# Performance work log

Hardware: AMD Instinct MI355X
Metric: run time of the kernel (lower is better)

## Reference

```python
import jax, jax.numpy as jnp
import numpy as np

N_GRAPHS = 256
NODES_PER_GRAPH = 64
N_NODES = N_GRAPHS * NODES_PER_GRAPH  # 16384
IN_F = 128
OUT_F = 128
N_HEADS = 16


def setup_inputs() -> dict:
    key = jax.random.key(0)
    k1, k2, k3, k4 = jax.random.split(key, 4)
    inputs = jax.random.normal(k1, (N_NODES, IN_F), dtype=jnp.float32)
    # fixed equal-sized graphs so sum(n_node) == N_NODES exactly
    n_node = jnp.full((N_GRAPHS,), NODES_PER_GRAPH, dtype=jnp.int32)
    head = jax.random.randint(k2, (N_GRAPHS,), 0, N_HEADS, dtype=jnp.int32)
    # lecun_normal-like init: std = 1/sqrt(fan_in)
    kernel = jax.random.normal(k3, (N_HEADS, IN_F, OUT_F), dtype=jnp.float32) * (1.0 / np.sqrt(IN_F))
    bias = jax.random.normal(k4, (N_HEADS, OUT_F), dtype=jnp.float32) * 0.02
    return {"inputs": inputs, "n_node": n_node, "head": head, "kernel": kernel, "bias": bias}


def reference(inputs, n_node, head, kernel, bias):
    # per-node head index: repeat each graph's head over its nodes
    node_head = jnp.repeat(head, n_node, total_repeat_length=inputs.shape[0])  # [N]
    k = kernel[node_head]                       # [N, in, out] (gathered per-node weights)
    y = jnp.einsum('bi,bio->bo', inputs, k)     # [N, out]
    y = y + bias[node_head]                     # [N, out]
    return y
```

## Files before the change

kernel.cpp:

```cpp
#include <hip/hip_runtime.h>
#include <hip/hip_bf16.h>

#define NG   256
#define NPG  64
#define INF  128
#define OUTF 128
#define NH   16

#define LDSK 136

typedef __attribute__((ext_vector_type(8))) short bf16x8;
typedef __attribute__((ext_vector_type(4))) float f32x4;

__device__ __forceinline__ ushort f2bf(float f) {
    union { float f; unsigned int i; } c; c.f = f;
    unsigned int r = c.i + 0x7fffu + ((c.i >> 16) & 1u);
    return (ushort)(r >> 16);
}

__global__ __launch_bounds__(512) void mhl_fused_kernel(
    const float* __restrict__ X,
    const int*   __restrict__ head,
    const float* __restrict__ W,
    const float* __restrict__ bias,
    float*       __restrict__ Y)
{
    __shared__ ushort Wl[OUTF * LDSK];

    int g = (int)blockIdx.x;
    int h = head[g];
    int t = (int)threadIdx.x;

    {
        int k  = t >> 2;
        int c0 = (t & 3) * 32;
        const float* src = W + h * (INF * OUTF) + k * OUTF + c0;
#pragma unroll
        for (int j = 0; j < 32; j += 4) {
            float4 v = *(const float4*)(src + j);
            Wl[(c0 + j + 0) * LDSK + k] = f2bf(v.x);
            Wl[(c0 + j + 1) * LDSK + k] = f2bf(v.y);
            Wl[(c0 + j + 2) * LDSK + k] = f2bf(v.z);
            Wl[(c0 + j + 3) * LDSK + k] = f2bf(v.w);
        }
    }
    __syncthreads();

    int wave = t >> 6;
    int lane = t & 63;
    int quad = lane >> 4;
    int l16  = lane & 15;

    int mrow = (wave & 3) * 16;
    int ncol = (wave >> 2) * 64;

    const float* Xg = X + (g * NPG + mrow + l16) * INF + quad * 8;
    bf16x8 a[4];
#pragma unroll
    for (int kt = 0; kt < 4; ++kt) {
        float v[8] __attribute__((aligned(16)));
        *(float4*)(&v[0]) = *(const float4*)(Xg + kt * 32);
        *(float4*)(&v[4]) = *(const float4*)(Xg + kt * 32 + 4);
#pragma unroll
        for (int j = 0; j < 8; ++j) a[kt][j] = (short)f2bf(v[j]);
    }

    f32x4 acc[4];
#pragma unroll
    for (int nt = 0; nt < 4; ++nt) acc[nt] = (f32x4){0.f, 0.f, 0.f, 0.f};

#pragma unroll
    for (int nt = 0; nt < 4; ++nt) {
        const ushort* Wn = &Wl[(ncol + nt * 16 + l16) * LDSK + quad * 8];
#pragma unroll
        for (int kt = 0; kt < 4; ++kt) {
            bf16x8 b = *(const bf16x8*)(Wn + kt * 32);
            acc[nt] = __builtin_amdgcn_mfma_f32_16x16x32_bf16(a[kt], b, acc[nt], 0, 0, 0);
        }
    }

    float* Yg = Y + (g * NPG + mrow) * OUTF + ncol;
#pragma unroll
    for (int nt = 0; nt < 4; ++nt) {
        float bv = bias[h * OUTF + ncol + nt * 16 + l16];
#pragma unroll
        for (int r = 0; r < 4; ++r)
            Yg[(quad * 4 + r) * OUTF + nt * 16 + l16] = acc[nt][r] + bv;
    }
}

extern "C" void kernel_launch(void* const* d_in, const int* in_sizes, int n_in,
                              void* d_out, int out_size, void* d_ws, size_t ws_size,
                              hipStream_t stream) {
    const float* X    = (const float*)d_in[0];
    const int*   head = (const int*)d_in[2];
    const float* W    = (const float*)d_in[3];
    const float* bias = (const float*)d_in[4];
    float* Y = (float*)d_out;

    mhl_fused_kernel<<<NG, 512, 0, stream>>>(X, head, W, bias, Y);
}
```

Before: 72.06 us.

## Split each graph across two blocks by output half and pack bf16 pairs in LDS

Each graph is now handled by two 256-thread blocks, each covering 64 output columns, so the grid doubles to 512 blocks and each block stages only half of the head's weight matrix. The weight staging now converts two adjacent k rows at once and writes packed 32-bit pairs to LDS, halving the number of LDS stores and reducing bank conflicts on the transposed writes. The aim is better CU occupancy on a GPU with many CUs and less per-block staging latency. The cost is that each block re-reads its X rows, so X is loaded twice per graph.

Measured after the change: 72.32 us. About the same (+0.4%).

```diff
diff --git a/kernel.cpp b/kernel.cpp
--- a/kernel.cpp
+++ b/kernel.cpp
@@ -18,30 +18,38 @@
     return (ushort)(r >> 16);
 }
 
-__global__ __launch_bounds__(512) void mhl_fused_kernel(
+__global__ __launch_bounds__(256) void mhl_fused_kernel(
     const float* __restrict__ X,
     const int*   __restrict__ head,
     const float* __restrict__ W,
     const float* __restrict__ bias,
     float*       __restrict__ Y)
 {
-    __shared__ ushort Wl[OUTF * LDSK];
+    __shared__ ushort Wl[64 * LDSK];
 
-    int g = (int)blockIdx.x;
-    int h = head[g];
-    int t = (int)threadIdx.x;
+    int bid = (int)blockIdx.x;
+    int g   = bid >> 1;
+    int c   = bid & 1;
+    int h   = head[g];
+    int t   = (int)threadIdx.x;
 
     {
-        int k  = t >> 2;
-        int c0 = (t & 3) * 32;
-        const float* src = W + h * (INF * OUTF) + k * OUTF + c0;
+        int kg  = t >> 2;
+        int ng  = t & 3;
+        int k0  = kg * 2;
+        int nn0 = ng * 16;
+        const float* s0 = W + h * (INF * OUTF) + k0 * OUTF + c * 64 + nn0;
+        const float* s1 = s0 + OUTF;
+        unsigned int* dst = (unsigned int*)Wl;
 #pragma unroll
-        for (int j = 0; j < 32; j += 4) {
-            float4 v = *(const float4*)(src + j);
-            Wl[(c0 + j + 0) * LDSK + k] = f2bf(v.x);
-            Wl[(c0 + j + 1) * LDSK + k] = f2bf(v.y);
-            Wl[(c0 + j + 2) * LDSK + k] = f2bf(v.z);
-            Wl[(c0 + j + 3) * LDSK + k] = f2bf(v.w);
+        for (int jj = 0; jj < 4; ++jj) {
+            float4 v0 = *(const float4*)(s0 + jj * 4);
+            float4 v1 = *(const float4*)(s1 + jj * 4);
+            int nn = nn0 + jj * 4;
+            dst[(nn + 0) * (LDSK / 2) + kg] = (unsigned int)f2bf(v0.x) | ((unsigned int)f2bf(v1.x) << 16);
+            dst[(nn + 1) * (LDSK / 2) + kg] = (unsigned int)f2bf(v0.y) | ((unsigned int)f2bf(v1.y) << 16);
+            dst[(nn + 2) * (LDSK / 2) + kg] = (unsigned int)f2bf(v0.z) | ((unsigned int)f2bf(v1.z) << 16);
+            dst[(nn + 3) * (LDSK / 2) + kg] = (unsigned int)f2bf(v0.w) | ((unsigned int)f2bf(v1.w) << 16);
         }
     }
     __syncthreads();
@@ -50,9 +58,7 @@
     int lane = t & 63;
     int quad = lane >> 4;
     int l16  = lane & 15;
-
-    int mrow = (wave & 3) * 16;
-    int ncol = (wave >> 2) * 64;
+    int mrow = wave * 16;
 
     const float* Xg = X + (g * NPG + mrow + l16) * INF + quad * 8;
     bf16x8 a[4];
@@ -71,7 +77,7 @@
 
 #pragma unroll
     for (int nt = 0; nt < 4; ++nt) {
-        const ushort* Wn = &Wl[(ncol + nt * 16 + l16) * LDSK + quad * 8];
+        const ushort* Wn = &Wl[(nt * 16 + l16) * LDSK + quad * 8];
 #pragma unroll
         for (int kt = 0; kt < 4; ++kt) {
             bf16x8 b = *(const bf16x8*)(Wn + kt * 32);
@@ -79,10 +85,10 @@
         }
     }
 
-    float* Yg = Y + (g * NPG + mrow) * OUTF + ncol;
+    float* Yg = Y + (g * NPG + mrow) * OUTF + c * 64;
 #pragma unroll
     for (int nt = 0; nt < 4; ++nt) {
-        float bv = bias[h * OUTF + ncol + nt * 16 + l16];
+        float bv = bias[h * OUTF + c * 64 + nt * 16 + l16];
 #pragma unroll
         for (int r = 0; r < 4; ++r)
             Yg[(quad * 4 + r) * OUTF + nt * 16 + l16] = acc[nt][r] + bv;
@@ -98,5 +104,5 @@
     const float* bias = (const float*)d_in[4];
     float* Y = (float*)d_out;
 
-    mhl_fused_kernel<<<NG, 512, 0, stream>>>(X, head, W, bias, Y);
+    mhl_fused_kernel<<<NG * 2, 256, 0, stream>>>(X, head, W, bias, Y);
 }
```
